# Kernel tuning notes

Hardware: AMD Instinct MI355X
Metric: run time of the kernel (lower is better)

Reference implementation:

```python
import jax, jax.numpy as jnp
import numpy as np

B, L, H = 4, 1024, 1024          # docs, seq_len, hidden (LUKE-large)
NH, M, E, R = 16, 64, 24, 512    # attn heads, mentions/doc, entities/doc, pairs/doc
EMB, BLK, NCLS = 768, 64, 97     # embed_size, block_size, num_class


def setup_inputs() -> dict:
    key = jax.random.key(0)
    ks = jax.random.split(key, 10)
    s = 0.02
    return {
        "seq_lhs": jax.random.normal(ks[0], (B, L, H), jnp.float32),
        "ent_lhs": jax.random.normal(ks[1], (B, M, H), jnp.float32),
        "ent_to_seq_attn": jax.random.uniform(ks[2], (B, NH, M, L), jnp.float32),
        "entity_id_labels": jax.random.randint(ks[3], (B, M), 0, E),
        "hts": jax.random.randint(ks[4], (B, R, 2), 0, E),
        "Wh": jax.random.normal(ks[5], (2 * H, EMB), jnp.float32) * s,
        "bh": jnp.zeros((EMB,), jnp.float32),
        "Wt": jax.random.normal(ks[6], (2 * H, EMB), jnp.float32) * s,
        "bt": jnp.zeros((EMB,), jnp.float32),
        "Wb": jax.random.normal(ks[7], (EMB * BLK, 768), jnp.float32) * s,
        "bb": jnp.zeros((768,), jnp.float32),
        "Wc": jax.random.normal(ks[8], (768, NCLS), jnp.float32) * s,
        "bc": jnp.zeros((NCLS,), jnp.float32),
    }


def reference(seq_lhs, ent_lhs, ent_to_seq_attn, entity_id_labels, hts,
              Wh, bh, Wt, bt, Wb, bb, Wc, bc):
    dt = seq_lhs.dtype
    # mention -> entity segment mask [B, E, M]
    mask = entity_id_labels[:, None, :] == jnp.arange(E)[None, :, None]
    counts = mask.sum(-1)  # [B, E]
    # entity embedding: logsumexp over its mentions (== identity for 1 mention),
    # zeros for entities with no mentions
    masked = jnp.where(mask[..., None], ent_lhs[:, None, :, :], jnp.asarray(-1e30, dt))
    ent_emb = jax.scipy.special.logsumexp(masked, axis=2)           # [B, E, H]
    ent_emb = jnp.where((counts > 0)[..., None], ent_emb, jnp.asarray(0.0, dt))
    # entity -> seq attention: mean over mentions, zeros for empty entities
    mf = mask.astype(dt)
    ent_attn = jnp.einsum('bem,bhml->behl', mf, ent_to_seq_attn)    # [B, E, NH, L]
    ent_attn = ent_attn / jnp.maximum(counts, 1)[:, :, None, None].astype(dt)
    # gather per-pair head/tail embeddings and attentions
    h_idx, t_idx = hts[..., 0], hts[..., 1]                          # [B, R]
    hs = jnp.take_along_axis(ent_emb, h_idx[..., None], axis=1)      # [B, R, H]
    ts = jnp.take_along_axis(ent_emb, t_idx[..., None], axis=1)
    ha = jnp.take_along_axis(ent_attn, h_idx[..., None, None], axis=1)  # [B, R, NH, L]
    ta = jnp.take_along_axis(ent_attn, t_idx[..., None, None], axis=1)
    ht = (ha * ta).mean(2)                                           # [B, R, L]
    ht = ht / (ht.sum(-1, keepdims=True) + 1e-5)
    rel = jnp.einsum('bld,brl->brd', seq_lhs, ht)                    # [B, R, H]
    # head/tail extractors with context concat
    he = jnp.tanh(jnp.concatenate([hs, rel], -1) @ Wh + bh)          # [B, R, EMB]
    te = jnp.tanh(jnp.concatenate([ts, rel], -1) @ Wt + bt)
    K = EMB // BLK
    b1 = he.reshape(B * R, K, BLK)
    b2 = te.reshape(B * R, K, BLK)
    bl = (b1[:, :, :, None] * b2[:, :, None, :]).reshape(B * R, EMB * BLK)
    embeds = bl @ Wb + bb                                            # [B*R, 768]
    return embeds @ Wc + bc                                          # [B*R, NCLS]
```

## Files before the change

kernel.cpp:

```cpp
#include <hip/hip_runtime.h>
#include <stdint.h>
#include <math.h>

#define B_    4
#define L_    1024
#define H_    1024
#define NH_   16
#define M_    64
#define E_    24
#define R_    512
#define EMB_  768
#define BLK_  64
#define NCLS_ 97
#define NR_   2048
#define KBIG_ 49152

typedef unsigned short ushort_t;
typedef unsigned int uint_t;
typedef short bf16x8 __attribute__((ext_vector_type(8)));
typedef float f32x4  __attribute__((ext_vector_type(4)));
typedef __bf16 bf16v2 __attribute__((ext_vector_type(2)));

__device__ __forceinline__ float bf2f(ushort_t u) {
    return __uint_as_float(((unsigned)u) << 16);
}
__device__ __forceinline__ ushort_t f2bf_rne(float f) {
    unsigned u = __float_as_uint(f);
    return (ushort_t)((u + 0x7fffu + ((u >> 16) & 1u)) >> 16);
}
__device__ __forceinline__ void cp16(const void* g, void* l) {
    __builtin_amdgcn_global_load_lds(
        (const __attribute__((address_space(1))) void*)g,
        (__attribute__((address_space(3))) void*)l, 16, 0, 0);
}

__global__ __launch_bounds__(256) void k_transpose_cvt(
    const float* __restrict__ in, ushort_t* __restrict__ out, int rows, int cols)
{
    __shared__ float t[64][65];
    int batch = blockIdx.z;
    in  += (size_t)batch * rows * cols;
    out += (size_t)batch * rows * cols;
    int c0 = blockIdx.x * 64, r0 = blockIdx.y * 64;
    int tx = threadIdx.x & 63, ty = threadIdx.x >> 6;
#pragma unroll
    for (int dr = 0; dr < 64; dr += 4)
        t[dr + ty][tx] = in[(size_t)(r0 + dr + ty) * cols + (c0 + tx)];
    __syncthreads();
    int c = threadIdx.x >> 2;
    int rk = (threadIdx.x & 3) * 16;
    ushort_t us[16];
#pragma unroll
    for (int q = 0; q < 16; q++) us[q] = f2bf_rne(t[rk + q][c]);
    ushort_t* op = &out[(size_t)(c0 + c) * rows + r0 + rk];
    *reinterpret_cast<int4*>(op)     = *reinterpret_cast<const int4*>(&us[0]);
    *reinterpret_cast<int4*>(op + 8) = *reinterpret_cast<const int4*>(&us[8]);
}

__global__ __launch_bounds__(256) void k_ent_emb(
    const float* __restrict__ ent_lhs, const int* __restrict__ labels,
    float* __restrict__ ent_emb)
{
    int b = blockIdx.x / E_, e = blockIdx.x % E_;
    __shared__ int list[M_];
    __shared__ int cnt;
    if (threadIdx.x == 0) cnt = 0;
    __syncthreads();
    if (threadIdx.x < M_ && labels[b * M_ + threadIdx.x] == e) {
        int p = atomicAdd(&cnt, 1);
        list[p] = threadIdx.x;
    }
    __syncthreads();
    int n = cnt;
    const float* base = ent_lhs + (size_t)b * M_ * H_;
    float* outp = ent_emb + ((size_t)b * E_ + e) * H_;
    for (int h = threadIdx.x; h < H_; h += blockDim.x) {
        if (n == 0) { outp[h] = 0.f; continue; }
        float mx = -1e30f;
        for (int i = 0; i < n; i++) mx = fmaxf(mx, base[(size_t)list[i] * H_ + h]);
        float s = 0.f;
        for (int i = 0; i < n; i++) s += __expf(base[(size_t)list[i] * H_ + h] - mx);
        outp[h] = mx + __logf(s);
    }
}

__global__ __launch_bounds__(256) void k_ent_attn(
    const float* __restrict__ attn, const int* __restrict__ labels,
    float* __restrict__ ent_attn)
{
    int idx = blockIdx.x;
    int nh = idx % NH_;
    int be = idx / NH_;
    int e = be % E_, b = be / E_;
    __shared__ int list[M_];
    __shared__ int cnt;
    if (threadIdx.x == 0) cnt = 0;
    __syncthreads();
    if (threadIdx.x < M_ && labels[b * M_ + threadIdx.x] == e) {
        int p = atomicAdd(&cnt, 1);
        list[p] = threadIdx.x;
    }
    __syncthreads();
    int n = cnt;
    float inv = 1.f / fmaxf((float)n, 1.f);
    const float* base = attn + ((size_t)b * NH_ + nh) * M_ * L_;
    float* outp = ent_attn + (((size_t)b * E_ + e) * NH_ + nh) * L_;
    for (int l = threadIdx.x; l < L_; l += blockDim.x) {
        float s = 0.f;
        for (int i = 0; i < n; i++) s += base[(size_t)list[i] * L_ + l];
        outp[l] = s * inv;
    }
}

__global__ __launch_bounds__(256) void k_ht(
    const float* __restrict__ ent_attn, const int* __restrict__ hts,
    ushort_t* __restrict__ ht_bf)
{
    int b = blockIdx.x / R_, r = blockIdx.x % R_;
    int h = hts[((size_t)b * R_ + r) * 2 + 0];
    int t = hts[((size_t)b * R_ + r) * 2 + 1];
    const float* ha = ent_attn + ((size_t)b * E_ + h) * NH_ * L_;
    const float* ta = ent_attn + ((size_t)b * E_ + t) * NH_ * L_;
    float vals[4];
    float local = 0.f;
#pragma unroll
    for (int p = 0; p < 4; p++) {
        int l = threadIdx.x + p * 256;
        float s = 0.f;
#pragma unroll
        for (int nh = 0; nh < NH_; nh++) s += ha[nh * L_ + l] * ta[nh * L_ + l];
        s *= (1.f / NH_);
        vals[p] = s;
        local += s;
    }
    __shared__ float red[4];
    float s = local;
#pragma unroll
    for (int off = 32; off > 0; off >>= 1) s += __shfl_down(s, off, 64);
    if ((threadIdx.x & 63) == 0) red[threadIdx.x >> 6] = s;
    __syncthreads();
    float tot = red[0] + red[1] + red[2] + red[3];
    float inv = 1.f / (tot + 1e-5f);
    ushort_t* outp = ht_bf + ((size_t)b * R_ + r) * L_;
#pragma unroll
    for (int p = 0; p < 4; p++) {
        int l = threadIdx.x + p * 256;
        outp[l] = f2bf_rne(vals[p] * inv);
    }
}

__global__ __launch_bounds__(256) void k_gather(
    const float* __restrict__ ent_emb, const int* __restrict__ hts,
    ushort_t* __restrict__ A1, ushort_t* __restrict__ A2)
{
    int n = blockIdx.x;
    int b = n / R_, r = n % R_;
    int h = hts[((size_t)b * R_ + r) * 2 + 0];
    int t = hts[((size_t)b * R_ + r) * 2 + 1];
    const float* eh = ent_emb + ((size_t)b * E_ + h) * H_;
    const float* et = ent_emb + ((size_t)b * E_ + t) * H_;
    for (int i = threadIdx.x; i < H_; i += 256) {
        A1[(size_t)n * 2048 + i] = f2bf_rne(eh[i]);
        A2[(size_t)n * 2048 + i] = f2bf_rne(et[i]);
    }
}

template <bool BIAS, bool TANH, bool DUAL>
__global__ __launch_bounds__(256) void k_gemm(
    const ushort_t* __restrict__ A, long sA, int lda,
    const ushort_t* __restrict__ Bt, long sB, int ldb,
    int K,
    const float* __restrict__ bias0, const float* __restrict__ bias1,
    ushort_t* __restrict__ C0, ushort_t* __restrict__ C1, long sC, int ldc)
{
    __shared__ ushort_t smem[2 * 128 * 72];
    ushort_t* As = smem;
    ushort_t* Bs = smem + 128 * 72;
    const int tid = threadIdx.x;
    const int lane = tid & 63, wid = tid >> 6;
    const int wr = wid >> 1, wc = wid & 1;
    const int z = blockIdx.z;
    const int m0 = blockIdx.y * 128, n0 = blockIdx.x * 128;
    A  += (long)z * sA;
    Bt += (long)z * sB;

    const f32x4 zero = {0.f, 0.f, 0.f, 0.f};
    f32x4 acc[4][4];
#pragma unroll
    for (int i = 0; i < 4; i++)
#pragma unroll
        for (int j = 0; j < 4; j++) acc[i][j] = zero;

    const int mrow = wr * 64 + (lane & 15);
    const int nrow = wc * 64 + (lane & 15);
    const int koff = (lane >> 4) * 8;

    for (int k0 = 0; k0 < K; k0 += 64) {
        __syncthreads();
#pragma unroll
        for (int p = 0; p < 4; p++) {
            int idx = tid + p * 256;
            int row = idx >> 3, seg = idx & 7;
            *reinterpret_cast<int4*>(&As[row * 72 + seg * 8]) =
                *reinterpret_cast<const int4*>(&A[(long)(m0 + row) * lda + k0 + seg * 8]);
            *reinterpret_cast<int4*>(&Bs[row * 72 + seg * 8]) =
                *reinterpret_cast<const int4*>(&Bt[(long)(n0 + row) * ldb + k0 + seg * 8]);
        }
        __syncthreads();
#pragma unroll
        for (int ks = 0; ks < 2; ks++) {
            bf16x8 af[4], bfg[4];
#pragma unroll
            for (int mt = 0; mt < 4; mt++)
                af[mt] = *reinterpret_cast<const bf16x8*>(&As[(mrow + mt * 16) * 72 + ks * 32 + koff]);
#pragma unroll
            for (int nt = 0; nt < 4; nt++)
                bfg[nt] = *reinterpret_cast<const bf16x8*>(&Bs[(nrow + nt * 16) * 72 + ks * 32 + koff]);
#pragma unroll
            for (int mt = 0; mt < 4; mt++)
#pragma unroll
                for (int nt = 0; nt < 4; nt++)
                    acc[mt][nt] = __builtin_amdgcn_mfma_f32_16x16x32_bf16(
                        af[mt], bfg[nt], acc[mt][nt], 0, 0, 0);
        }
    }

    const float* bias = BIAS ? (z ? bias1 : bias0) : nullptr;
    __syncthreads();
#pragma unroll
    for (int mt = 0; mt < 4; mt++) {
#pragma unroll
        for (int nt = 0; nt < 4; nt++) {
#pragma unroll
            for (int rg = 0; rg < 4; rg++) {
                int row = wr * 64 + mt * 16 + (lane >> 4) * 4 + rg;
                int col = wc * 64 + nt * 16 + (lane & 15);
                float v = acc[mt][nt][rg];
                if (BIAS) v += bias[n0 + col];
                if (TANH) {
                    float vc = fminf(fmaxf(v, -15.f), 15.f);
                    float ex = __expf(2.f * vc);
                    v = (ex - 1.f) / (ex + 1.f);
                }
                smem[row * 132 + col] = f2bf_rne(v);
            }
        }
    }
    __syncthreads();
    {
        int row = tid >> 1, half = tid & 1;
        const ushort_t* src = &smem[row * 132 + half * 64];
        ushort_t* dst0 = &C0[(long)z * sC + (long)(m0 + row) * ldc + n0 + half * 64];
#pragma unroll
        for (int q = 0; q < 8; q++)
            *reinterpret_cast<int4*>(dst0 + q * 8) = *reinterpret_cast<const int4*>(src + q * 8);
        if (DUAL) {
            ushort_t* dst1 = &C1[(long)z * sC + (long)(m0 + row) * ldc + n0 + half * 64];
#pragma unroll
            for (int q = 0; q < 8; q++)
                *reinterpret_cast<int4*>(dst1 + q * 8) = *reinterpret_cast<const int4*>(src + q * 8);
        }
    }
}

__global__ __launch_bounds__(256, 3) void k_bilinear(
    const ushort_t* __restrict__ he, const ushort_t* __restrict__ te,
    const ushort_t* __restrict__ Wbt, float* __restrict__ embedsN, int slices)
{
    __shared__ ushort_t HEs[128 * 72];
    __shared__ ushort_t Bsh[2][128 * 64];
    const int tid = threadIdx.x;
    const int lane = tid & 63, wid = tid >> 6;
    const int wr = wid >> 1, wc = wid & 1;
    const int bid = blockIdx.x;
    const int z = bid & 7;
    const int w = bid >> 3;
    const int d0 = (w % 6) * 128, n0 = (w / 6) * 128;
    const int c0 = z * 96, cend = c0 + 96;

    const f32x4 zero = {0.f, 0.f, 0.f, 0.f};
    f32x4 acc[4][4];
#pragma unroll
    for (int i = 0; i < 4; i++)
#pragma unroll
        for (int j = 0; j < 4; j++) acc[i][j] = zero;

    const int r15 = lane & 15;
    const int q4 = lane >> 4;
    const int mrow = wr * 64 + r15;
    const int koff = q4 * 8;

    const ushort_t* Pg = Wbt
        + (long)(d0 + wid * 32 + (lane >> 3)) * KBIG_
        + ((lane & 7) ^ ((lane >> 3) & 7)) * 8;

    int c = c0;
    while (c < cend) {
        const int kk = c >> 6;
        const int i0 = c & 63;
        const int i1 = min(64, i0 + (cend - c));

        __syncthreads();

        {
            const ushort_t* g = Pg + (long)(kk * 64 + i0) * 64;
            ushort_t* Pl = Bsh[0] + wid * 2048;
            cp16(g,              Pl);
            cp16(g +  8 * KBIG_, Pl + 512);
            cp16(g + 16 * KBIG_, Pl + 1024);
            cp16(g + 24 * KBIG_, Pl + 1536);
        }

#pragma unroll
        for (int p = 0; p < 4; p++) {
            int idx = tid + p * 256;
            int row = idx >> 3, seg = idx & 7;
            *reinterpret_cast<int4*>(&HEs[row * 72 + seg * 8]) =
                *reinterpret_cast<const int4*>(&he[(long)(n0 + row) * EMB_ + kk * 64 + seg * 8]);
        }
        __syncthreads();

        float tf[4][2][8];
#pragma unroll
        for (int mt = 0; mt < 4; mt++)
#pragma unroll
            for (int ks = 0; ks < 2; ks++) {
                uint4 t = *reinterpret_cast<const uint4*>(
                    &te[(long)(n0 + mrow + mt * 16) * EMB_ + kk * 64 + ks * 32 + koff]);
                const ushort_t* ts = reinterpret_cast<const ushort_t*>(&t);
#pragma unroll
                for (int qq = 0; qq < 8; qq++) tf[mt][ks][qq] = bf2f(ts[qq]);
            }

        int cur = 0;
        for (int i = i0; i < i1; i++) {
            if (i + 1 < i1) {
                const ushort_t* g = Pg + (long)(kk * 64 + i + 1) * 64;
                ushort_t* Pl = Bsh[cur ^ 1] + wid * 2048;
                cp16(g,              Pl);
                cp16(g +  8 * KBIG_, Pl + 512);
                cp16(g + 16 * KBIG_, Pl + 1024);
                cp16(g + 24 * KBIG_, Pl + 1536);
                asm volatile("s_waitcnt vmcnt(4)" ::: "memory");
            } else {
                asm volatile("s_waitcnt vmcnt(0)" ::: "memory");
            }
            __builtin_amdgcn_s_barrier();
            __builtin_amdgcn_sched_barrier(0);

            const ushort_t* Bcur = Bsh[cur];
            bf16x8 bfr[2][4];
#pragma unroll
            for (int ks = 0; ks < 2; ks++) {
                const int segoff = (((ks * 4 + q4) ^ (r15 & 7)) * 8);
#pragma unroll
                for (int nt = 0; nt < 4; nt++)
                    bfr[ks][nt] = *reinterpret_cast<const bf16x8*>(
                        &Bcur[(wc * 64 + nt * 16 + r15) * 64 + segoff]);
            }
#pragma unroll
            for (int mt = 0; mt < 4; mt++) {
                float hf = bf2f(HEs[(mrow + mt * 16) * 72 + i]);
#pragma unroll
                for (int ks = 0; ks < 2; ks++) {
                    union { __bf16 h[8]; bf16x8 v; } af;
#pragma unroll
                    for (int qq = 0; qq < 8; qq++)
                        af.h[qq] = (__bf16)(tf[mt][ks][qq] * hf);
#pragma unroll
                    for (int nt = 0; nt < 4; nt++)
                        acc[mt][nt] = __builtin_amdgcn_mfma_f32_16x16x32_bf16(
                            af.v, bfr[ks][nt], acc[mt][nt], 0, 0, 0);
                }
            }
            __builtin_amdgcn_s_barrier();
            __builtin_amdgcn_sched_barrier(0);
            cur ^= 1;
        }
        c += (i1 - i0);
    }

    float* outp = embedsN + (slices == 8 ? (long)z * NR_ * EMB_ : 0l);
    const bool plain = (slices == 8);
#pragma unroll
    for (int mt = 0; mt < 4; mt++)
#pragma unroll
        for (int nt = 0; nt < 4; nt++)
#pragma unroll
            for (int rg = 0; rg < 4; rg++) {
                int n = n0 + wr * 64 + mt * 16 + q4 * 4 + rg;
                int d = d0 + wc * 64 + nt * 16 + r15;
                if (plain) outp[(long)n * EMB_ + d] = acc[mt][nt][rg];
                else       atomicAdd(&outp[(long)n * EMB_ + d], acc[mt][nt][rg]);
            }
}

__global__ __launch_bounds__(128) void k_final(
    const float* __restrict__ embedsN, int nz, const float* __restrict__ bb,
    const float* __restrict__ Wc, const float* __restrict__ bc,
    float* __restrict__ out)
{
    int n = blockIdx.x;
    __shared__ float row[EMB_];
    for (int i = threadIdx.x; i < EMB_; i += 128) {
        float s = bb[i];
        for (int zz = 0; zz < nz; zz++)
            s += embedsN[(size_t)zz * NR_ * EMB_ + (size_t)n * EMB_ + i];
        row[i] = s;
    }
    __syncthreads();
    int j = threadIdx.x;
    if (j < NCLS_) {
        float s = bc[j];
#pragma unroll 8
        for (int d = 0; d < EMB_; d++) s += row[d] * Wc[d * NCLS_ + j];
        out[(size_t)n * NCLS_ + j] = s;
    }
}

extern "C" void kernel_launch(void* const* d_in, const int* in_sizes, int n_in,
                              void* d_out, int out_size, void* d_ws, size_t ws_size,
                              hipStream_t stream)
{
    (void)in_sizes; (void)n_in; (void)out_size;
    const float* seq    = (const float*)d_in[0];
    const float* entl   = (const float*)d_in[1];
    const float* attn   = (const float*)d_in[2];
    const int*   labels = (const int*)d_in[3];
    const int*   hts    = (const int*)d_in[4];
    const float* Wh     = (const float*)d_in[5];
    const float* bh     = (const float*)d_in[6];
    const float* Wt     = (const float*)d_in[7];
    const float* bt     = (const float*)d_in[8];
    const float* Wb     = (const float*)d_in[9];
    const float* bb     = (const float*)d_in[10];
    const float* Wc     = (const float*)d_in[11];
    const float* bc     = (const float*)d_in[12];
    float* out = (float*)d_out;

    char* ws = (char*)d_ws;
    size_t off = 0;
    auto alloc = [&](size_t bytes) -> char* {
        char* p = ws + off;
        off += (bytes + 255) & ~(size_t)255;
        return p;
    };
    float*    ent_emb  = (float*)alloc((size_t)B_ * E_ * H_ * 4);
    float*    ent_attn = (float*)alloc((size_t)B_ * E_ * NH_ * L_ * 4);
    ushort_t* ht_bf    = (ushort_t*)alloc((size_t)B_ * R_ * L_ * 2);
    ushort_t* seq_t    = (ushort_t*)alloc((size_t)B_ * H_ * L_ * 2);
    ushort_t* A1       = (ushort_t*)alloc((size_t)NR_ * 2048 * 2);
    ushort_t* A2       = (ushort_t*)alloc((size_t)NR_ * 2048 * 2);
    ushort_t* Whb      = (ushort_t*)alloc((size_t)EMB_ * 2048 * 2);
    ushort_t* Wtb      = (ushort_t*)alloc((size_t)EMB_ * 2048 * 2);
    ushort_t* he_bf    = (ushort_t*)alloc((size_t)NR_ * EMB_ * 2);
    ushort_t* te_bf    = (ushort_t*)alloc((size_t)NR_ * EMB_ * 2);
    ushort_t* Wbt      = (ushort_t*)alloc((size_t)EMB_ * KBIG_ * 2);

    const size_t slice_b = (size_t)NR_ * EMB_ * 4;
    int slices = (ws_size >= off + 8 * slice_b) ? 8 : 1;
    float* embedsN = (float*)alloc((size_t)slices * slice_b);

    k_transpose_cvt<<<dim3(H_ / 64, L_ / 64, B_), 256, 0, stream>>>(seq, seq_t, L_, H_);
    k_transpose_cvt<<<dim3(EMB_ / 64, 2048 / 64, 1), 256, 0, stream>>>(Wh, Whb, 2048, EMB_);
    k_transpose_cvt<<<dim3(EMB_ / 64, 2048 / 64, 1), 256, 0, stream>>>(Wt, Wtb, 2048, EMB_);
    k_transpose_cvt<<<dim3(EMB_ / 64, KBIG_ / 64, 1), 256, 0, stream>>>(Wb, Wbt, KBIG_, EMB_);

    k_ent_emb<<<B_ * E_, 256, 0, stream>>>(entl, labels, ent_emb);
    k_ent_attn<<<B_ * E_ * NH_, 256, 0, stream>>>(attn, labels, ent_attn);

    k_ht<<<NR_, 256, 0, stream>>>(ent_attn, hts, ht_bf);
    k_gather<<<NR_, 256, 0, stream>>>(ent_emb, hts, A1, A2);

    k_gemm<false, false, true><<<dim3(H_ / 128, R_ / 128, B_), 256, 0, stream>>>(
        ht_bf, (long)R_ * L_, L_,
        seq_t, (long)H_ * L_, L_,
        L_, nullptr, nullptr,
        A1 + 1024, A2 + 1024, (long)R_ * 2048, 2048);

    k_gemm<true, true, false><<<dim3(EMB_ / 128, NR_ / 128, 2), 256, 0, stream>>>(
        A1, (long)NR_ * 2048, 2048,
        Whb, (long)EMB_ * 2048, 2048,
        2048, bh, bt,
        he_bf, nullptr, (long)NR_ * EMB_, EMB_);

    if (slices == 1)
        (void)hipMemsetAsync(embedsN, 0, slice_b, stream);
    k_bilinear<<<768, 256, 0, stream>>>(he_bf, te_bf, Wbt, embedsN, slices);

    k_final<<<NR_, 128, 0, stream>>>(embedsN, slices, bb, Wc, bc, out);
}
```

Measured before the change: 636.9 us.

## Load bilinear weight fragments directly into registers instead of via LDS

The bilinear kernel no longer stages Wb tiles through double-buffered shared memory with async global-to-LDS copies and per-column barriers. Each wave now loads its own MFMA B fragments straight from global memory into registers, ping-ponging between two register buffers to overlap loads with compute. This removes the LDS round trip and two barriers per column. In exchange it uses more registers (occupancy hint lowered to 2), issues less coalesced 16-byte global loads, and assumes the column count per chunk is even.

```diff
diff --git a/kernel.cpp b/kernel.cpp
--- a/kernel.cpp
+++ b/kernel.cpp
@@ -19,7 +19,6 @@
 typedef unsigned int uint_t;
 typedef short bf16x8 __attribute__((ext_vector_type(8)));
 typedef float f32x4  __attribute__((ext_vector_type(4)));
-typedef __bf16 bf16v2 __attribute__((ext_vector_type(2)));
 
 __device__ __forceinline__ float bf2f(ushort_t u) {
     return __uint_as_float(((unsigned)u) << 16);
@@ -27,11 +26,6 @@
 __device__ __forceinline__ ushort_t f2bf_rne(float f) {
     unsigned u = __float_as_uint(f);
     return (ushort_t)((u + 0x7fffu + ((u >> 16) & 1u)) >> 16);
-}
-__device__ __forceinline__ void cp16(const void* g, void* l) {
-    __builtin_amdgcn_global_load_lds(
-        (const __attribute__((address_space(1))) void*)g,
-        (__attribute__((address_space(3))) void*)l, 16, 0, 0);
 }
 
 __global__ __launch_bounds__(256) void k_transpose_cvt(
@@ -263,12 +257,11 @@
     }
 }
 
-__global__ __launch_bounds__(256, 3) void k_bilinear(
+__global__ __launch_bounds__(256, 2) void k_bilinear(
     const ushort_t* __restrict__ he, const ushort_t* __restrict__ te,
     const ushort_t* __restrict__ Wbt, float* __restrict__ embedsN, int slices)
 {
     __shared__ ushort_t HEs[128 * 72];
-    __shared__ ushort_t Bsh[2][128 * 64];
     const int tid = threadIdx.x;
     const int lane = tid & 63, wid = tid >> 6;
     const int wr = wid >> 1, wc = wid & 1;
@@ -290,9 +283,42 @@
     const int mrow = wr * 64 + r15;
     const int koff = q4 * 8;
 
-    const ushort_t* Pg = Wbt
-        + (long)(d0 + wid * 32 + (lane >> 3)) * KBIG_
-        + ((lane & 7) ^ ((lane >> 3) & 7)) * 8;
+    const ushort_t* Brow0 = Wbt + (long)(d0 + wc * 64 + 0 * 16 + r15) * KBIG_ + koff;
+    const ushort_t* Brow1 = Wbt + (long)(d0 + wc * 64 + 1 * 16 + r15) * KBIG_ + koff;
+    const ushort_t* Brow2 = Wbt + (long)(d0 + wc * 64 + 2 * 16 + r15) * KBIG_ + koff;
+    const ushort_t* Brow3 = Wbt + (long)(d0 + wc * 64 + 3 * 16 + r15) * KBIG_ + koff;
+
+    uint4 bA[8], bB[8];
+    float tf[4][2][8];
+
+    auto loadB = [&](uint4* bx, int col) {
+        const long cb = (long)col * 64;
+#pragma unroll
+        for (int ks = 0; ks < 2; ks++) {
+            bx[ks * 4 + 0] = *reinterpret_cast<const uint4*>(Brow0 + cb + ks * 32);
+            bx[ks * 4 + 1] = *reinterpret_cast<const uint4*>(Brow1 + cb + ks * 32);
+            bx[ks * 4 + 2] = *reinterpret_cast<const uint4*>(Brow2 + cb + ks * 32);
+            bx[ks * 4 + 3] = *reinterpret_cast<const uint4*>(Brow3 + cb + ks * 32);
+        }
+    };
+    auto compute = [&](const uint4* bx, int i) {
+#pragma unroll
+        for (int mt = 0; mt < 4; mt++) {
+            float hf = bf2f(HEs[(mrow + mt * 16) * 72 + i]);
+#pragma unroll
+            for (int ks = 0; ks < 2; ks++) {
+                union { __bf16 h[8]; bf16x8 v; } af;
+#pragma unroll
+                for (int qq = 0; qq < 8; qq++)
+                    af.h[qq] = (__bf16)(tf[mt][ks][qq] * hf);
+#pragma unroll
+                for (int nt = 0; nt < 4; nt++)
+                    acc[mt][nt] = __builtin_amdgcn_mfma_f32_16x16x32_bf16(
+                        af.v, *reinterpret_cast<const bf16x8*>(&bx[ks * 4 + nt]),
+                        acc[mt][nt], 0, 0, 0);
+            }
+        }
+    };
 
     int c = c0;
     while (c < cend) {
@@ -301,16 +327,6 @@
         const int i1 = min(64, i0 + (cend - c));
 
         __syncthreads();
-
-        {
-            const ushort_t* g = Pg + (long)(kk * 64 + i0) * 64;
-            ushort_t* Pl = Bsh[0] + wid * 2048;
-            cp16(g,              Pl);
-            cp16(g +  8 * KBIG_, Pl + 512);
-            cp16(g + 16 * KBIG_, Pl + 1024);
-            cp16(g + 24 * KBIG_, Pl + 1536);
-        }
-
 #pragma unroll
         for (int p = 0; p < 4; p++) {
             int idx = tid + p * 256;
@@ -320,7 +336,6 @@
         }
         __syncthreads();
 
-        float tf[4][2][8];
 #pragma unroll
         for (int mt = 0; mt < 4; mt++)
 #pragma unroll
@@ -332,50 +347,12 @@
                 for (int qq = 0; qq < 8; qq++) tf[mt][ks][qq] = bf2f(ts[qq]);
             }
 
-        int cur = 0;
-        for (int i = i0; i < i1; i++) {
-            if (i + 1 < i1) {
-                const ushort_t* g = Pg + (long)(kk * 64 + i + 1) * 64;
-                ushort_t* Pl = Bsh[cur ^ 1] + wid * 2048;
-                cp16(g,              Pl);
-                cp16(g +  8 * KBIG_, Pl + 512);
-                cp16(g + 16 * KBIG_, Pl + 1024);
-                cp16(g + 24 * KBIG_, Pl + 1536);
-                asm volatile("s_waitcnt vmcnt(4)" ::: "memory");
-            } else {
-                asm volatile("s_waitcnt vmcnt(0)" ::: "memory");
-            }
-            __builtin_amdgcn_s_barrier();
-            __builtin_amdgcn_sched_barrier(0);
-
-            const ushort_t* Bcur = Bsh[cur];
-            bf16x8 bfr[2][4];
-#pragma unroll
-            for (int ks = 0; ks < 2; ks++) {
-                const int segoff = (((ks * 4 + q4) ^ (r15 & 7)) * 8);
-#pragma unroll
-                for (int nt = 0; nt < 4; nt++)
-                    bfr[ks][nt] = *reinterpret_cast<const bf16x8*>(
-                        &Bcur[(wc * 64 + nt * 16 + r15) * 64 + segoff]);
-            }
-#pragma unroll
-            for (int mt = 0; mt < 4; mt++) {
-                float hf = bf2f(HEs[(mrow + mt * 16) * 72 + i]);
-#pragma unroll
-                for (int ks = 0; ks < 2; ks++) {
-                    union { __bf16 h[8]; bf16x8 v; } af;
-#pragma unroll
-                    for (int qq = 0; qq < 8; qq++)
-                        af.h[qq] = (__bf16)(tf[mt][ks][qq] * hf);
-#pragma unroll
-                    for (int nt = 0; nt < 4; nt++)
-                        acc[mt][nt] = __builtin_amdgcn_mfma_f32_16x16x32_bf16(
-                            af.v, bfr[ks][nt], acc[mt][nt], 0, 0, 0);
-                }
-            }
-            __builtin_amdgcn_s_barrier();
-            __builtin_amdgcn_sched_barrier(0);
-            cur ^= 1;
+        loadB(bA, kk * 64 + i0);
+        for (int i = i0; i < i1; i += 2) {
+            loadB(bB, kk * 64 + i + 1);
+            compute(bA, i);
+            if (i + 2 < i1) loadB(bA, kk * 64 + i + 2);
+            compute(bB, i + 1);
         }
         c += (i1 - i0);
     }
```

Result: slower. 746.9 us (+17.3%).
